# Optimization experiments

Hardware: AMD Instinct MI355X
Metric: run time of the kernel (lower is better)

Reference implementation:

```python
import jax, jax.numpy as jnp
import numpy as np

DIM = 384
HEADS = 6
N_TOKEN = 2240
HIDDEN = int(DIM * 4.0)
EPS = 1e-5


def layernorm(x, g, b):
    mu = jnp.mean(x, axis=-1, keepdims=True)
    var = jnp.mean(jnp.square(x - mu), axis=-1, keepdims=True)
    return (x - mu) * jax.lax.rsqrt(var + EPS) * g + b


def setup_inputs() -> dict:
    key = jax.random.key(0)
    ks = jax.random.split(key, 10)
    B, N, C = 2, 2240, DIM
    s = 0.02
    return {
        "x": jax.random.normal(ks[0], (B, N, C), dtype=jnp.float32),
        "encoder_pos": jax.random.normal(ks[1], (1, N_TOKEN, C), dtype=jnp.float32) * s,
        "ln1_g": jnp.ones((C,), jnp.float32),
        "ln1_b": jnp.zeros((C,), jnp.float32),
        "w_qkv": jax.random.normal(ks[2], (3 * C, C), dtype=jnp.float32) * s,  # torch Linear [out,in], no bias
        "w_proj": jax.random.normal(ks[3], (C, C), dtype=jnp.float32) * s,
        "b_proj": jnp.zeros((C,), jnp.float32),
        "ln2_g": jnp.ones((C,), jnp.float32),
        "ln2_b": jnp.zeros((C,), jnp.float32),
        "w_fc1": jax.random.normal(ks[4], (HIDDEN, C), dtype=jnp.float32) * s,
        "b_fc1": jnp.zeros((HIDDEN,), jnp.float32),
        "w_fc2": jax.random.normal(ks[5], (C, HIDDEN), dtype=jnp.float32) * s,
        "b_fc2": jnp.zeros((C,), jnp.float32),
    }


def reference(x, encoder_pos, ln1_g, ln1_b, w_qkv, w_proj, b_proj, ln2_g, ln2_b, w_fc1, b_fc1, w_fc2, b_fc2):
    B, N, C = x.shape
    H = HEADS
    hd = C // H
    scale = hd ** -0.5

    # positional embedding: each of the n_token rows repeated N//n_token times (contiguously)
    rep = N // encoder_pos.shape[1]
    pos = jnp.repeat(encoder_pos, rep, axis=1)  # [1, N, C]
    x = x + pos

    # attention
    h = layernorm(x, ln1_g, ln1_b)
    qkv = h @ w_qkv.T  # [B, N, 3C]
    qkv = qkv.reshape(B, N, 3, H, hd).transpose(2, 0, 3, 1, 4)  # [3, B, H, N, hd]
    q, k, v = qkv[0], qkv[1], qkv[2]
    attn = jax.nn.softmax(jnp.einsum("bhqd,bhkd->bhqk", q, k) * scale, axis=-1)  # [B, H, N, N]
    o = jnp.einsum("bhqk,bhkd->bhqd", attn, v).transpose(0, 2, 1, 3).reshape(B, N, C)
    o = o @ w_proj.T + b_proj
    x = x + o

    # MLP
    h = layernorm(x, ln2_g, ln2_b)
    h = jax.nn.gelu(h @ w_fc1.T + b_fc1, approximate=False)
    h = h @ w_fc2.T + b_fc2
    x = x + h
    return (x, attn)
```

## Files before the change

### kernel.cpp

```cpp
#include <hip/hip_runtime.h>
#include <math.h>

typedef unsigned short u16;
typedef unsigned int   u32;
typedef __attribute__((ext_vector_type(8))) short short8;
typedef __attribute__((ext_vector_type(4))) float floatx4;

#define MFMA16(a,b,c) __builtin_amdgcn_mfma_f32_16x16x32_bf16((a),(b),(c),0,0,0)

constexpr int BB  = 2;
constexpr int NT  = 2240;
constexpr int CD  = 384;
constexpr int NH  = 6;
constexpr int HD  = 64;
constexpr int HID = 1536;
constexpr int M   = BB * NT;
constexpr int CS  = 5;
constexpr int CTILES = NT / 64 / CS;
constexpr float SCALE = 0.125f;

__device__ inline u16 f2bf(float f) {
  u32 u = __float_as_uint(f);
  u = (u + 0x7fffu + ((u >> 16) & 1u)) >> 16;
  return (u16)u;
}
__device__ inline float bf2f(u16 b) { return __uint_as_float(((u32)b) << 16); }

__global__ void cvt_all(const float* __restrict__ s0, u16* __restrict__ d0, int n0_,
                        const float* __restrict__ s1, u16* __restrict__ d1, int n1_,
                        const float* __restrict__ s2, u16* __restrict__ d2, int n2_,
                        const float* __restrict__ s3, u16* __restrict__ d3, int n3_) {
  int i = (blockIdx.x * 256 + threadIdx.x) * 4;
  const float* s; u16* d; int base;
  if (i < n0_)                   { s = s0; d = d0; base = 0; }
  else if (i < n0_ + n1_)        { s = s1; d = d1; base = n0_; }
  else if (i < n0_ + n1_ + n2_)  { s = s2; d = d2; base = n0_ + n1_; }
  else                           { s = s3; d = d3; base = n0_ + n1_ + n2_; }
  int j = i - base;
  float4 v = *(const float4*)(s + j);
  ushort4 o; o.x = f2bf(v.x); o.y = f2bf(v.y); o.z = f2bf(v.z); o.w = f2bf(v.w);
  *(ushort4*)(d + j) = o;
}

__global__ __launch_bounds__(128) void ln_kernel(
    const float* __restrict__ xin, const float* __restrict__ pos,
    const float* __restrict__ g, const float* __restrict__ bta,
    float* __restrict__ x1out, u16* __restrict__ hout) {
  int row = blockIdx.x;
  int n = row % NT;
  int t = threadIdx.x;
  const float* xr = xin + (size_t)row * CD;
  float v[3], s1 = 0.f, s2 = 0.f;
  #pragma unroll
  for (int j = 0; j < 3; ++j) {
    int c = t + j * 128;
    float x = xr[c];
    if (pos) x += pos[(size_t)n * CD + c];
    v[j] = x; s1 += x; s2 += x * x;
  }
  #pragma unroll
  for (int off = 32; off; off >>= 1) { s1 += __shfl_down(s1, off); s2 += __shfl_down(s2, off); }
  __shared__ float rbuf[4];
  __shared__ float stats[2];
  int lane = t & 63, wid = t >> 6;
  if (lane == 0) { rbuf[wid] = s1; rbuf[2 + wid] = s2; }
  __syncthreads();
  if (t == 0) {
    float a = rbuf[0] + rbuf[1], b2 = rbuf[2] + rbuf[3];
    float mu = a / CD;
    float var = b2 / CD - mu * mu;
    stats[0] = mu; stats[1] = rsqrtf(var + 1e-5f);
  }
  __syncthreads();
  float mu = stats[0], rs = stats[1];
  #pragma unroll
  for (int j = 0; j < 3; ++j) {
    int c = t + j * 128;
    float h = (v[j] - mu) * rs * g[c] + bta[c];
    hout[(size_t)row * CD + c] = f2bf(h);
    if (x1out) x1out[(size_t)row * CD + c] = v[j];
  }
}

template <int EPI>
__global__ __launch_bounds__(256) void gemm_bt(
    const u16* __restrict__ A, const u16* __restrict__ Wt, int K,
    const float* __restrict__ bias, const float* __restrict__ res,
    float* __restrict__ outf, u16* __restrict__ outb,
    u16* __restrict__ qout, u16* __restrict__ kout, u16* __restrict__ vtout) {
  __shared__ __align__(16) u16 As[64][72];
  __shared__ __align__(16) u16 Bs[64][72];
  int m0 = blockIdx.y * 64, n0 = blockIdx.x * 64;
  int t = threadIdx.x;
  int lane = t & 63, w = t >> 6, wm = w & 1, wn = w >> 1;
  int quad = lane >> 4, c16 = lane & 15;
  int lrow = t >> 2, lseg = t & 3;
  const u16* ga = A + (size_t)(m0 + lrow) * K + lseg * 8;
  const u16* gb = Wt + (size_t)(n0 + lrow) * K + lseg * 8;
  floatx4 acc[2][2] = {};
  for (int k0 = 0; k0 < K; k0 += 64) {
    uint4 av0 = *(const uint4*)(ga + k0);
    uint4 av1 = *(const uint4*)(ga + k0 + 32);
    uint4 bv0 = *(const uint4*)(gb + k0);
    uint4 bv1 = *(const uint4*)(gb + k0 + 32);
    __syncthreads();
    *(uint4*)&As[lrow][lseg * 8] = av0;
    *(uint4*)&As[lrow][32 + lseg * 8] = av1;
    *(uint4*)&Bs[lrow][lseg * 8] = bv0;
    *(uint4*)&Bs[lrow][32 + lseg * 8] = bv1;
    __syncthreads();
    #pragma unroll
    for (int ks = 0; ks < 2; ++ks) {
      short8 af[2], bf[2];
      #pragma unroll
      for (int mt = 0; mt < 2; ++mt) af[mt] = *(const short8*)&As[wm * 32 + mt * 16 + c16][ks * 32 + quad * 8];
      #pragma unroll
      for (int nt = 0; nt < 2; ++nt) bf[nt] = *(const short8*)&Bs[wn * 32 + nt * 16 + c16][ks * 32 + quad * 8];
      #pragma unroll
      for (int mt = 0; mt < 2; ++mt)
        #pragma unroll
        for (int nt = 0; nt < 2; ++nt)
          acc[mt][nt] = MFMA16(af[mt], bf[nt], acc[mt][nt]);
    }
  }
  if (EPI == 0) {
    int s = n0 / 384;
    int hh = (n0 % 384) / 64;
    int b_ = m0 / NT, nn0 = m0 % NT;
    __syncthreads();
    #pragma unroll
    for (int mt = 0; mt < 2; ++mt)
      #pragma unroll
      for (int nt = 0; nt < 2; ++nt)
        #pragma unroll
        for (int r = 0; r < 4; ++r) {
          int m_l = wm * 32 + mt * 16 + quad * 4 + r;
          int d_l = wn * 32 + nt * 16 + c16;
          u16 bv = f2bf(acc[mt][nt][r]);
          if (s < 2) As[m_l][d_l] = bv;
          else       As[d_l][m_l] = bv;
        }
    __syncthreads();
    int row = t >> 2, cs0 = (t & 3) * 16;
    uint4 va = *(const uint4*)&As[row][cs0];
    uint4 vb = *(const uint4*)&As[row][cs0 + 8];
    u16* dst;
    if (s == 0)      dst = qout  + ((size_t)(b_ * NH + hh) * NT + nn0 + row) * HD + cs0;
    else if (s == 1) dst = kout  + ((size_t)(b_ * NH + hh) * NT + nn0 + row) * HD + cs0;
    else             dst = vtout + ((size_t)(b_ * NH + hh) * HD + row) * NT + nn0 + cs0;
    *(uint4*)dst = va;
    *(uint4*)(dst + 8) = vb;
  } else {
    #pragma unroll
    for (int mt = 0; mt < 2; ++mt) {
      #pragma unroll
      for (int nt = 0; nt < 2; ++nt) {
        int rg0 = m0 + wm * 32 + mt * 16 + quad * 4;
        int cg = n0 + wn * 32 + nt * 16 + c16;
        #pragma unroll
        for (int r = 0; r < 4; ++r) {
          float v = acc[mt][nt][r];
          int m = rg0 + r;
          if (EPI == 2) {
            v += bias[cg];
            v = 0.5f * v * (1.0f + erff(v * 0.70710678118f));
            outb[(size_t)m * HID + cg] = f2bf(v);
          } else {
            outf[(size_t)m * CD + cg] = v + bias[cg] + res[(size_t)m * CD + cg];
          }
        }
      }
    }
  }
}

__global__ __launch_bounds__(256) void attn_pass1(
    const u16* __restrict__ qb, const u16* __restrict__ kb, float* __restrict__ ml) {
  __shared__ __align__(16) u16 Ks[64][72];
  int bh = blockIdx.y, chunk = blockIdx.z;
  int q0 = blockIdx.x * 64;
  int t = threadIdx.x, w = t >> 6, lane = t & 63, quad = lane >> 4, c16 = lane & 15;
  int lrow = t >> 2, lseg = t & 3;

  const u16* qp = qb + ((size_t)bh * NT + q0 + w * 16 + c16) * HD;
  short8 qf0 = *(const short8*)(qp + quad * 8);
  short8 qf1 = *(const short8*)(qp + 32 + quad * 8);
  const u16* kbase = kb + (size_t)bh * NT * HD;

  float m_i[4], l_i[4];
  #pragma unroll
  for (int r = 0; r < 4; ++r) { m_i[r] = -1e30f; l_i[r] = 0.f; }

  for (int ct = 0; ct < CTILES; ++ct) {
    int col0 = (chunk * CTILES + ct) * 64;
    const u16* kg = kbase + (size_t)(col0 + lrow) * HD + lseg * 8;
    uint4 kv0 = *(const uint4*)kg;
    uint4 kv1 = *(const uint4*)(kg + 32);
    __syncthreads();
    *(uint4*)&Ks[lrow][lseg * 8] = kv0;
    *(uint4*)&Ks[lrow][32 + lseg * 8] = kv1;
    __syncthreads();
    floatx4 s_acc[4] = {};
    #pragma unroll
    for (int nt = 0; nt < 4; ++nt) {
      const u16* kp = &Ks[nt * 16 + c16][quad * 8];
      s_acc[nt] = MFMA16(qf0, *(const short8*)(kp), s_acc[nt]);
      s_acc[nt] = MFMA16(qf1, *(const short8*)(kp + 32), s_acc[nt]);
    }
    #pragma unroll
    for (int r = 0; r < 4; ++r) {
      float rm = fmaxf(fmaxf(s_acc[0][r], s_acc[1][r]), fmaxf(s_acc[2][r], s_acc[3][r])) * SCALE;
      #pragma unroll
      for (int off = 1; off < 16; off <<= 1) rm = fmaxf(rm, __shfl_xor(rm, off));
      float nm = fmaxf(m_i[r], rm);
      float ps = 0.f;
      #pragma unroll
      for (int nt = 0; nt < 4; ++nt) ps += __expf(s_acc[nt][r] * SCALE - nm);
      #pragma unroll
      for (int off = 1; off < 16; off <<= 1) ps += __shfl_xor(ps, off);
      l_i[r] = l_i[r] * __expf(m_i[r] - nm) + ps;
      m_i[r] = nm;
    }
  }
  if (c16 == 0) {
    #pragma unroll
    for (int r = 0; r < 4; ++r) {
      int row = q0 + w * 16 + quad * 4 + r;
      float* p = ml + ((size_t)(bh * NT + row) * CS + chunk) * 2;
      p[0] = m_i[r]; p[1] = l_i[r];
    }
  }
}

__global__ __launch_bounds__(256) void attn_pass2(
    const u16* __restrict__ qb, const u16* __restrict__ kb, const u16* __restrict__ vtb,
    const float* __restrict__ ml, float* __restrict__ attn_out, u16* __restrict__ o_part) {
  __shared__ __align__(16) u16 Ks[64][72];
  __shared__ __align__(16) u16 Vs[64][72];
  __shared__ __align__(16) u16 Plds[4][16][72];
  __shared__ float mfin[64], rlfin[64];
  int bh = blockIdx.y, chunk = blockIdx.z;
  int b = bh / NH, hh = bh % NH;
  int q0 = blockIdx.x * 64;
  int t = threadIdx.x, w = t >> 6, lane = t & 63, quad = lane >> 4, c16 = lane & 15;
  int lrow = t >> 2, lseg = t & 3;

  if (t < 64) {
    const float* p = ml + (size_t)(bh * NT + q0 + t) * CS * 2;
    float mm = -1e30f;
    #pragma unroll
    for (int c = 0; c < CS; ++c) mm = fmaxf(mm, p[c * 2]);
    float ll = 0.f;
    #pragma unroll
    for (int c = 0; c < CS; ++c) ll += p[c * 2 + 1] * __expf(p[c * 2] - mm);
    mfin[t] = mm; rlfin[t] = 1.0f / ll;
  }
  __syncthreads();
  float m_i[4], rl[4];
  #pragma unroll
  for (int r = 0; r < 4; ++r) {
    int rr = w * 16 + quad * 4 + r;
    m_i[r] = mfin[rr]; rl[r] = rlfin[rr];
  }

  const u16* qp = qb + ((size_t)bh * NT + q0 + w * 16 + c16) * HD;
  short8 qf0 = *(const short8*)(qp + quad * 8);
  short8 qf1 = *(const short8*)(qp + 32 + quad * 8);
  const u16* kbase = kb + (size_t)bh * NT * HD;
  const u16* vbase = vtb + (size_t)bh * HD * NT;

  floatx4 o_acc[4] = {};
  float* attn_bh = attn_out + (size_t)bh * NT * NT;
  for (int ct = 0; ct < CTILES; ++ct) {
    int col0 = (chunk * CTILES + ct) * 64;
    const u16* kg = kbase + (size_t)(col0 + lrow) * HD + lseg * 8;
    const u16* vg = vbase + (size_t)lrow * NT + col0 + lseg * 8;
    uint4 kv0 = *(const uint4*)kg;
    uint4 kv1 = *(const uint4*)(kg + 32);
    uint4 vv0 = *(const uint4*)vg;
    uint4 vv1 = *(const uint4*)(vg + 32);
    __syncthreads();
    *(uint4*)&Ks[lrow][lseg * 8] = kv0;
    *(uint4*)&Ks[lrow][32 + lseg * 8] = kv1;
    *(uint4*)&Vs[lrow][lseg * 8] = vv0;
    *(uint4*)&Vs[lrow][32 + lseg * 8] = vv1;
    __syncthreads();
    floatx4 s_acc[4] = {};
    #pragma unroll
    for (int nt = 0; nt < 4; ++nt) {
      const u16* kp = &Ks[nt * 16 + c16][quad * 8];
      s_acc[nt] = MFMA16(qf0, *(const short8*)(kp), s_acc[nt]);
      s_acc[nt] = MFMA16(qf1, *(const short8*)(kp + 32), s_acc[nt]);
    }
    #pragma unroll
    for (int nt = 0; nt < 4; ++nt) {
      #pragma unroll
      for (int r = 0; r < 4; ++r) {
        float p = __expf(s_acc[nt][r] * SCALE - m_i[r]) * rl[r];
        __builtin_nontemporal_store(
            p, &attn_bh[(size_t)(q0 + w * 16 + quad * 4 + r) * NT + col0 + nt * 16 + c16]);
        Plds[w][quad * 4 + r][nt * 16 + c16] = f2bf(p);
      }
    }
    #pragma unroll
    for (int ks = 0; ks < 2; ++ks) {
      short8 pa = *(const short8*)&Plds[w][c16][ks * 32 + quad * 8];
      #pragma unroll
      for (int dt = 0; dt < 4; ++dt) {
        short8 vb = *(const short8*)&Vs[dt * 16 + c16][ks * 32 + quad * 8];
        o_acc[dt] = MFMA16(pa, vb, o_acc[dt]);
      }
    }
  }
  #pragma unroll
  for (int dt = 0; dt < 4; ++dt) {
    #pragma unroll
    for (int r = 0; r < 4; ++r) {
      int m = b * NT + q0 + w * 16 + quad * 4 + r;
      int cc = hh * 64 + dt * 16 + c16;
      o_part[((size_t)chunk * M + m) * CD + cc] = f2bf(o_acc[dt][r]);
    }
  }
}

__global__ void osum_kernel(const u16* __restrict__ o_part, u16* __restrict__ o_bf) {
  int i = (blockIdx.x * 256 + threadIdx.x) * 4;
  float4 s = {0.f, 0.f, 0.f, 0.f};
  #pragma unroll
  for (int c = 0; c < CS; ++c) {
    ushort4 v = *(const ushort4*)(o_part + (size_t)c * M * CD + i);
    s.x += bf2f(v.x); s.y += bf2f(v.y); s.z += bf2f(v.z); s.w += bf2f(v.w);
  }
  ushort4 o; o.x = f2bf(s.x); o.y = f2bf(s.y); o.z = f2bf(s.z); o.w = f2bf(s.w);
  *(ushort4*)(o_bf + i) = o;
}

extern "C" void kernel_launch(void* const* d_in, const int* in_sizes, int n_in,
                              void* d_out, int out_size, void* d_ws, size_t ws_size,
                              hipStream_t stream) {
  const float* x      = (const float*)d_in[0];
  const float* pos    = (const float*)d_in[1];
  const float* ln1_g  = (const float*)d_in[2];
  const float* ln1_b  = (const float*)d_in[3];
  const float* w_qkv  = (const float*)d_in[4];
  const float* w_proj = (const float*)d_in[5];
  const float* b_proj = (const float*)d_in[6];
  const float* ln2_g  = (const float*)d_in[7];
  const float* ln2_b  = (const float*)d_in[8];
  const float* w_fc1  = (const float*)d_in[9];
  const float* b_fc1  = (const float*)d_in[10];
  const float* w_fc2  = (const float*)d_in[11];
  const float* b_fc2  = (const float*)d_in[12];

  float* out      = (float*)d_out;
  float* attn_out = out + (size_t)M * CD;

  char* ws = (char*)d_ws;
  size_t o = 0;
  auto carve = [&](size_t bytes) { char* p = ws + o; o += bytes; return p; };
  float* x1    = (float*)carve((size_t)M * CD * 4);
  u16* h1      = (u16*)carve((size_t)M * CD * 2);
  u16* wqkv_b  = (u16*)carve((size_t)3 * CD * CD * 2);
  u16* wproj_b = (u16*)carve((size_t)CD * CD * 2);
  u16* wfc1_b  = (u16*)carve((size_t)HID * CD * 2);
  u16* wfc2_b  = (u16*)carve((size_t)CD * HID * 2);
  u16* q_bf    = (u16*)carve((size_t)BB * NH * NT * HD * 2);
  u16* k_bf    = (u16*)carve((size_t)BB * NH * NT * HD * 2);
  u16* vt_bf   = (u16*)carve((size_t)BB * NH * NT * HD * 2);
  u16* o_bf    = (u16*)carve((size_t)M * CD * 2);
  float* x2    = (float*)carve((size_t)M * CD * 4);
  u16* h2      = (u16*)carve((size_t)M * CD * 2);
  u16* g_bf    = (u16*)carve((size_t)M * HID * 2);
  float* ml    = (float*)carve((size_t)NH * BB * NT * CS * 2 * 4);
  u16* o_part  = (u16*)carve((size_t)CS * M * CD * 2);
  (void)ws_size; (void)in_sizes; (void)n_in; (void)out_size;

  constexpr int NQ = 3 * CD * CD, NP = CD * CD, N1 = HID * CD, N2 = CD * HID;
  cvt_all<<<(NQ + NP + N1 + N2) / 1024, 256, 0, stream>>>(
      w_qkv, wqkv_b, NQ, w_proj, wproj_b, NP, w_fc1, wfc1_b, N1, w_fc2, wfc2_b, N2);

  ln_kernel<<<M, 128, 0, stream>>>(x, pos, ln1_g, ln1_b, x1, h1);

  gemm_bt<0><<<dim3((3 * CD) / 64, M / 64), 256, 0, stream>>>(
      h1, wqkv_b, CD, nullptr, nullptr, nullptr, nullptr, q_bf, k_bf, vt_bf);

  attn_pass1<<<dim3(NT / 64, BB * NH, CS), 256, 0, stream>>>(q_bf, k_bf, ml);
  attn_pass2<<<dim3(NT / 64, BB * NH, CS), 256, 0, stream>>>(q_bf, k_bf, vt_bf, ml, attn_out, o_part);
  osum_kernel<<<(M * CD) / 1024, 256, 0, stream>>>(o_part, o_bf);

  gemm_bt<3><<<dim3(CD / 64, M / 64), 256, 0, stream>>>(
      o_bf, wproj_b, CD, b_proj, x1, x2, nullptr, nullptr, nullptr, nullptr);
  ln_kernel<<<M, 128, 0, stream>>>(x2, nullptr, ln2_g, ln2_b, nullptr, h2);

  gemm_bt<2><<<dim3(HID / 64, M / 64), 256, 0, stream>>>(
      h2, wfc1_b, CD, b_fc1, nullptr, nullptr, g_bf, nullptr, nullptr, nullptr);

  gemm_bt<3><<<dim3(CD / 64, M / 64), 256, 0, stream>>>(
      g_bf, wfc2_b, HID, b_fc2, x2, out, nullptr, nullptr, nullptr, nullptr);
}
```

Measured before the change: 430.6 us.

## Fuse weight conversion into LN, fold partial-O sum into proj GEMM, prefetch tiles

Merges the weight fp32-to-bf16 conversion into the first layernorm launch as extra blocks. Removes the separate partial-output summation kernel by summing the five attention chunk partials inside the projection GEMM's A-tile load. Adds register prefetch of the next K/V or A/B tile in the GEMM and both attention passes. Pass1 swaps MFMA operand order so each lane holds a single query row's statistics, cutting the shuffle reductions. These changes remove launches and a memory round trip, at the cost of five times the A loads and more register pressure in the projection GEMM.

```diff
diff --git a/kernel.cpp b/kernel.cpp
--- a/kernel.cpp
+++ b/kernel.cpp
@@ -26,28 +26,82 @@
 }
 __device__ inline float bf2f(u16 b) { return __uint_as_float(((u32)b) << 16); }
 
-__global__ void cvt_all(const float* __restrict__ s0, u16* __restrict__ d0, int n0_,
-                        const float* __restrict__ s1, u16* __restrict__ d1, int n1_,
-                        const float* __restrict__ s2, u16* __restrict__ d2, int n2_,
-                        const float* __restrict__ s3, u16* __restrict__ d3, int n3_) {
-  int i = (blockIdx.x * 256 + threadIdx.x) * 4;
-  const float* s; u16* d; int base;
-  if (i < n0_)                   { s = s0; d = d0; base = 0; }
-  else if (i < n0_ + n1_)        { s = s1; d = d1; base = n0_; }
-  else if (i < n0_ + n1_ + n2_)  { s = s2; d = d2; base = n0_ + n1_; }
-  else                           { s = s3; d = d3; base = n0_ + n1_ + n2_; }
-  int j = i - base;
-  float4 v = *(const float4*)(s + j);
-  ushort4 o; o.x = f2bf(v.x); o.y = f2bf(v.y); o.z = f2bf(v.z); o.w = f2bf(v.w);
-  *(ushort4*)(d + j) = o;
-}
-
-__global__ __launch_bounds__(128) void ln_kernel(
+__device__ inline uint4 sum5_bf(uint4 a0, uint4 a1, uint4 a2, uint4 a3, uint4 a4) {
+  union U { uint4 v; u16 h[8]; };
+  U u0, u1, u2, u3, u4, o;
+  u0.v = a0; u1.v = a1; u2.v = a2; u3.v = a3; u4.v = a4;
+  #pragma unroll
+  for (int e = 0; e < 8; ++e) {
+    float f = bf2f(u0.h[e]) + bf2f(u1.h[e]) + bf2f(u2.h[e]) + bf2f(u3.h[e]) + bf2f(u4.h[e]);
+    o.h[e] = f2bf(f);
+  }
+  return o.v;
+}
+
+constexpr int NQ = 3 * CD * CD, NP = CD * CD, N1 = HID * CD, N2 = CD * HID;
+constexpr int CVT_BLOCKS = (NQ + NP + N1 + N2) / 512;
+
+__global__ __launch_bounds__(128) void ln_cvt_kernel(
     const float* __restrict__ xin, const float* __restrict__ pos,
     const float* __restrict__ g, const float* __restrict__ bta,
-    float* __restrict__ x1out, u16* __restrict__ hout) {
+    float* __restrict__ x1out, u16* __restrict__ hout,
+    const float* __restrict__ s0, u16* __restrict__ d0,
+    const float* __restrict__ s1, u16* __restrict__ d1,
+    const float* __restrict__ s2, u16* __restrict__ d2,
+    const float* __restrict__ s3, u16* __restrict__ d3) {
+  int t = threadIdx.x;
+  if (blockIdx.x >= M) {
+    int i = ((blockIdx.x - M) * 128 + t) * 4;
+    const float* s; u16* d; int base;
+    if (i < NQ)                { s = s0; d = d0; base = 0; }
+    else if (i < NQ + NP)      { s = s1; d = d1; base = NQ; }
+    else if (i < NQ + NP + N1) { s = s2; d = d2; base = NQ + NP; }
+    else                       { s = s3; d = d3; base = NQ + NP + N1; }
+    int j = i - base;
+    float4 v = *(const float4*)(s + j);
+    ushort4 o; o.x = f2bf(v.x); o.y = f2bf(v.y); o.z = f2bf(v.z); o.w = f2bf(v.w);
+    *(ushort4*)(d + j) = o;
+    return;
+  }
   int row = blockIdx.x;
   int n = row % NT;
+  const float* xr = xin + (size_t)row * CD;
+  float v[3], s1v = 0.f, s2v = 0.f;
+  #pragma unroll
+  for (int j = 0; j < 3; ++j) {
+    int c = t + j * 128;
+    float x = xr[c] + pos[(size_t)n * CD + c];
+    v[j] = x; s1v += x; s2v += x * x;
+  }
+  #pragma unroll
+  for (int off = 32; off; off >>= 1) { s1v += __shfl_down(s1v, off); s2v += __shfl_down(s2v, off); }
+  __shared__ float rbuf[4];
+  __shared__ float stats[2];
+  int lane = t & 63, wid = t >> 6;
+  if (lane == 0) { rbuf[wid] = s1v; rbuf[2 + wid] = s2v; }
+  __syncthreads();
+  if (t == 0) {
+    float a = rbuf[0] + rbuf[1], b2 = rbuf[2] + rbuf[3];
+    float mu = a / CD;
+    float var = b2 / CD - mu * mu;
+    stats[0] = mu; stats[1] = rsqrtf(var + 1e-5f);
+  }
+  __syncthreads();
+  float mu = stats[0], rs = stats[1];
+  #pragma unroll
+  for (int j = 0; j < 3; ++j) {
+    int c = t + j * 128;
+    float h = (v[j] - mu) * rs * g[c] + bta[c];
+    hout[(size_t)row * CD + c] = f2bf(h);
+    x1out[(size_t)row * CD + c] = v[j];
+  }
+}
+
+__global__ __launch_bounds__(128) void ln_kernel(
+    const float* __restrict__ xin,
+    const float* __restrict__ g, const float* __restrict__ bta,
+    u16* __restrict__ hout) {
+  int row = blockIdx.x;
   int t = threadIdx.x;
   const float* xr = xin + (size_t)row * CD;
   float v[3], s1 = 0.f, s2 = 0.f;
@@ -55,7 +109,6 @@
   for (int j = 0; j < 3; ++j) {
     int c = t + j * 128;
     float x = xr[c];
-    if (pos) x += pos[(size_t)n * CD + c];
     v[j] = x; s1 += x; s2 += x * x;
   }
   #pragma unroll
@@ -76,13 +129,11 @@
   #pragma unroll
   for (int j = 0; j < 3; ++j) {
     int c = t + j * 128;
-    float h = (v[j] - mu) * rs * g[c] + bta[c];
-    hout[(size_t)row * CD + c] = f2bf(h);
-    if (x1out) x1out[(size_t)row * CD + c] = v[j];
-  }
-}
-
-template <int EPI>
+    hout[(size_t)row * CD + c] = f2bf((v[j] - mu) * rs * g[c] + bta[c]);
+  }
+}
+
+template <int EPI, bool OSUM>
 __global__ __launch_bounds__(256) void gemm_bt(
     const u16* __restrict__ A, const u16* __restrict__ Wt, int K,
     const float* __restrict__ bias, const float* __restrict__ res,
@@ -95,20 +146,39 @@
   int lane = t & 63, w = t >> 6, wm = w & 1, wn = w >> 1;
   int quad = lane >> 4, c16 = lane & 15;
   int lrow = t >> 2, lseg = t & 3;
-  const u16* ga = A + (size_t)(m0 + lrow) * K + lseg * 8;
+  constexpr int SL = OSUM ? 5 : 1;
+  const u16* ga[SL];
+  #pragma unroll
+  for (int s = 0; s < SL; ++s)
+    ga[s] = A + (size_t)s * M * CD + (size_t)(m0 + lrow) * K + lseg * 8;
   const u16* gb = Wt + (size_t)(n0 + lrow) * K + lseg * 8;
   floatx4 acc[2][2] = {};
+  uint4 av0[SL], av1[SL], bv0, bv1;
+  #pragma unroll
+  for (int s = 0; s < SL; ++s) { av0[s] = *(const uint4*)(ga[s]); av1[s] = *(const uint4*)(ga[s] + 32); }
+  bv0 = *(const uint4*)(gb);
+  bv1 = *(const uint4*)(gb + 32);
   for (int k0 = 0; k0 < K; k0 += 64) {
-    uint4 av0 = *(const uint4*)(ga + k0);
-    uint4 av1 = *(const uint4*)(ga + k0 + 32);
-    uint4 bv0 = *(const uint4*)(gb + k0);
-    uint4 bv1 = *(const uint4*)(gb + k0 + 32);
-    __syncthreads();
-    *(uint4*)&As[lrow][lseg * 8] = av0;
-    *(uint4*)&As[lrow][32 + lseg * 8] = av1;
+    __syncthreads();
+    uint4 wa0, wa1;
+    if (OSUM) {
+      wa0 = sum5_bf(av0[0], av0[1], av0[2], av0[3], av0[4 % SL]);
+      wa1 = sum5_bf(av1[0], av1[1], av1[2], av1[3], av1[4 % SL]);
+    } else { wa0 = av0[0]; wa1 = av1[0]; }
+    *(uint4*)&As[lrow][lseg * 8] = wa0;
+    *(uint4*)&As[lrow][32 + lseg * 8] = wa1;
     *(uint4*)&Bs[lrow][lseg * 8] = bv0;
     *(uint4*)&Bs[lrow][32 + lseg * 8] = bv1;
     __syncthreads();
+    if (k0 + 64 < K) {
+      #pragma unroll
+      for (int s = 0; s < SL; ++s) {
+        av0[s] = *(const uint4*)(ga[s] + k0 + 64);
+        av1[s] = *(const uint4*)(ga[s] + k0 + 96);
+      }
+      bv0 = *(const uint4*)(gb + k0 + 64);
+      bv1 = *(const uint4*)(gb + k0 + 96);
+    }
     #pragma unroll
     for (int ks = 0; ks < 2; ++ks) {
       short8 af[2], bf[2];
@@ -187,48 +257,52 @@
   short8 qf1 = *(const short8*)(qp + 32 + quad * 8);
   const u16* kbase = kb + (size_t)bh * NT * HD;
 
-  float m_i[4], l_i[4];
-  #pragma unroll
-  for (int r = 0; r < 4; ++r) { m_i[r] = -1e30f; l_i[r] = 0.f; }
+  float m_i = -1e30f, l_i = 0.f;
+
+  const u16* kg = kbase + (size_t)(chunk * CTILES * 64 + lrow) * HD + lseg * 8;
+  uint4 kv0 = *(const uint4*)kg;
+  uint4 kv1 = *(const uint4*)(kg + 32);
 
   for (int ct = 0; ct < CTILES; ++ct) {
-    int col0 = (chunk * CTILES + ct) * 64;
-    const u16* kg = kbase + (size_t)(col0 + lrow) * HD + lseg * 8;
-    uint4 kv0 = *(const uint4*)kg;
-    uint4 kv1 = *(const uint4*)(kg + 32);
     __syncthreads();
     *(uint4*)&Ks[lrow][lseg * 8] = kv0;
     *(uint4*)&Ks[lrow][32 + lseg * 8] = kv1;
     __syncthreads();
+    if (ct + 1 < CTILES) {
+      const u16* kn = kbase + (size_t)((chunk * CTILES + ct + 1) * 64 + lrow) * HD + lseg * 8;
+      kv0 = *(const uint4*)kn;
+      kv1 = *(const uint4*)(kn + 32);
+    }
     floatx4 s_acc[4] = {};
     #pragma unroll
     for (int nt = 0; nt < 4; ++nt) {
       const u16* kp = &Ks[nt * 16 + c16][quad * 8];
-      s_acc[nt] = MFMA16(qf0, *(const short8*)(kp), s_acc[nt]);
-      s_acc[nt] = MFMA16(qf1, *(const short8*)(kp + 32), s_acc[nt]);
-    }
-    #pragma unroll
-    for (int r = 0; r < 4; ++r) {
-      float rm = fmaxf(fmaxf(s_acc[0][r], s_acc[1][r]), fmaxf(s_acc[2][r], s_acc[3][r])) * SCALE;
-      #pragma unroll
-      for (int off = 1; off < 16; off <<= 1) rm = fmaxf(rm, __shfl_xor(rm, off));
-      float nm = fmaxf(m_i[r], rm);
-      float ps = 0.f;
-      #pragma unroll
-      for (int nt = 0; nt < 4; ++nt) ps += __expf(s_acc[nt][r] * SCALE - nm);
-      #pragma unroll
-      for (int off = 1; off < 16; off <<= 1) ps += __shfl_xor(ps, off);
-      l_i[r] = l_i[r] * __expf(m_i[r] - nm) + ps;
-      m_i[r] = nm;
-    }
-  }
-  if (c16 == 0) {
-    #pragma unroll
-    for (int r = 0; r < 4; ++r) {
-      int row = q0 + w * 16 + quad * 4 + r;
-      float* p = ml + ((size_t)(bh * NT + row) * CS + chunk) * 2;
-      p[0] = m_i[r]; p[1] = l_i[r];
-    }
+      s_acc[nt] = MFMA16(*(const short8*)(kp), qf0, s_acc[nt]);
+      s_acc[nt] = MFMA16(*(const short8*)(kp + 32), qf1, s_acc[nt]);
+    }
+    float rm = -1e30f;
+    #pragma unroll
+    for (int nt = 0; nt < 4; ++nt)
+      #pragma unroll
+      for (int r = 0; r < 4; ++r) rm = fmaxf(rm, s_acc[nt][r]);
+    rm *= SCALE;
+    rm = fmaxf(rm, __shfl_xor(rm, 16));
+    rm = fmaxf(rm, __shfl_xor(rm, 32));
+    float nm = fmaxf(m_i, rm);
+    float ps = 0.f;
+    #pragma unroll
+    for (int nt = 0; nt < 4; ++nt)
+      #pragma unroll
+      for (int r = 0; r < 4; ++r) ps += __expf(s_acc[nt][r] * SCALE - nm);
+    ps += __shfl_xor(ps, 16);
+    ps += __shfl_xor(ps, 32);
+    l_i = l_i * __expf(m_i - nm) + ps;
+    m_i = nm;
+  }
+  if (quad == 0) {
+    int row = q0 + w * 16 + c16;
+    float* p = ml + ((size_t)(bh * NT + row) * CS + chunk) * 2;
+    p[0] = m_i; p[1] = l_i;
   }
 }
 
@@ -245,6 +319,17 @@
   int t = threadIdx.x, w = t >> 6, lane = t & 63, quad = lane >> 4, c16 = lane & 15;
   int lrow = t >> 2, lseg = t & 3;
 
+  const u16* kbase = kb + (size_t)bh * NT * HD;
+  const u16* vbase = vtb + (size_t)bh * HD * NT;
+
+  int col00 = chunk * CTILES * 64;
+  const u16* kg = kbase + (size_t)(col00 + lrow) * HD + lseg * 8;
+  const u16* vg = vbase + (size_t)lrow * NT + col00 + lseg * 8;
+  uint4 kv0 = *(const uint4*)kg;
+  uint4 kv1 = *(const uint4*)(kg + 32);
+  uint4 vv0 = *(const uint4*)vg;
+  uint4 vv1 = *(const uint4*)(vg + 32);
+
   if (t < 64) {
     const float* p = ml + (size_t)(bh * NT + q0 + t) * CS * 2;
     float mm = -1e30f;
@@ -266,25 +351,26 @@
   const u16* qp = qb + ((size_t)bh * NT + q0 + w * 16 + c16) * HD;
   short8 qf0 = *(const short8*)(qp + quad * 8);
   short8 qf1 = *(const short8*)(qp + 32 + quad * 8);
-  const u16* kbase = kb + (size_t)bh * NT * HD;
-  const u16* vbase = vtb + (size_t)bh * HD * NT;
 
   floatx4 o_acc[4] = {};
   float* attn_bh = attn_out + (size_t)bh * NT * NT;
   for (int ct = 0; ct < CTILES; ++ct) {
     int col0 = (chunk * CTILES + ct) * 64;
-    const u16* kg = kbase + (size_t)(col0 + lrow) * HD + lseg * 8;
-    const u16* vg = vbase + (size_t)lrow * NT + col0 + lseg * 8;
-    uint4 kv0 = *(const uint4*)kg;
-    uint4 kv1 = *(const uint4*)(kg + 32);
-    uint4 vv0 = *(const uint4*)vg;
-    uint4 vv1 = *(const uint4*)(vg + 32);
     __syncthreads();
     *(uint4*)&Ks[lrow][lseg * 8] = kv0;
     *(uint4*)&Ks[lrow][32 + lseg * 8] = kv1;
     *(uint4*)&Vs[lrow][lseg * 8] = vv0;
     *(uint4*)&Vs[lrow][32 + lseg * 8] = vv1;
     __syncthreads();
+    if (ct + 1 < CTILES) {
+      int coln = col0 + 64;
+      const u16* kn = kbase + (size_t)(coln + lrow) * HD + lseg * 8;
+      const u16* vn = vbase + (size_t)lrow * NT + coln + lseg * 8;
+      kv0 = *(const uint4*)kn;
+      kv1 = *(const uint4*)(kn + 32);
+      vv0 = *(const uint4*)vn;
+      vv1 = *(const uint4*)(vn + 32);
+    }
     floatx4 s_acc[4] = {};
     #pragma unroll
     for (int nt = 0; nt < 4; ++nt) {
@@ -321,18 +407,6 @@
       o_part[((size_t)chunk * M + m) * CD + cc] = f2bf(o_acc[dt][r]);
     }
   }
-}
-
-__global__ void osum_kernel(const u16* __restrict__ o_part, u16* __restrict__ o_bf) {
-  int i = (blockIdx.x * 256 + threadIdx.x) * 4;
-  float4 s = {0.f, 0.f, 0.f, 0.f};
-  #pragma unroll
-  for (int c = 0; c < CS; ++c) {
-    ushort4 v = *(const ushort4*)(o_part + (size_t)c * M * CD + i);
-    s.x += bf2f(v.x); s.y += bf2f(v.y); s.z += bf2f(v.z); s.w += bf2f(v.w);
-  }
-  ushort4 o; o.x = f2bf(s.x); o.y = f2bf(s.y); o.z = f2bf(s.z); o.w = f2bf(s.w);
-  *(ushort4*)(o_bf + i) = o;
 }
 
 extern "C" void kernel_launch(void* const* d_in, const int* in_sizes, int n_in,
@@ -367,7 +441,6 @@
   u16* q_bf    = (u16*)carve((size_t)BB * NH * NT * HD * 2);
   u16* k_bf    = (u16*)carve((size_t)BB * NH * NT * HD * 2);
   u16* vt_bf   = (u16*)carve((size_t)BB * NH * NT * HD * 2);
-  u16* o_bf    = (u16*)carve((size_t)M * CD * 2);
   float* x2    = (float*)carve((size_t)M * CD * 4);
   u16* h2      = (u16*)carve((size_t)M * CD * 2);
   u16* g_bf    = (u16*)carve((size_t)M * HID * 2);
@@ -375,26 +448,23 @@
   u16* o_part  = (u16*)carve((size_t)CS * M * CD * 2);
   (void)ws_size; (void)in_sizes; (void)n_in; (void)out_size;
 
-  constexpr int NQ = 3 * CD * CD, NP = CD * CD, N1 = HID * CD, N2 = CD * HID;
-  cvt_all<<<(NQ + NP + N1 + N2) / 1024, 256, 0, stream>>>(
-      w_qkv, wqkv_b, NQ, w_proj, wproj_b, NP, w_fc1, wfc1_b, N1, w_fc2, wfc2_b, N2);
-
-  ln_kernel<<<M, 128, 0, stream>>>(x, pos, ln1_g, ln1_b, x1, h1);
-
-  gemm_bt<0><<<dim3((3 * CD) / 64, M / 64), 256, 0, stream>>>(
+  ln_cvt_kernel<<<M + CVT_BLOCKS, 128, 0, stream>>>(
+      x, pos, ln1_g, ln1_b, x1, h1,
+      w_qkv, wqkv_b, w_proj, wproj_b, w_fc1, wfc1_b, w_fc2, wfc2_b);
+
+  gemm_bt<0, false><<<dim3((3 * CD) / 64, M / 64), 256, 0, stream>>>(
       h1, wqkv_b, CD, nullptr, nullptr, nullptr, nullptr, q_bf, k_bf, vt_bf);
 
   attn_pass1<<<dim3(NT / 64, BB * NH, CS), 256, 0, stream>>>(q_bf, k_bf, ml);
   attn_pass2<<<dim3(NT / 64, BB * NH, CS), 256, 0, stream>>>(q_bf, k_bf, vt_bf, ml, attn_out, o_part);
-  osum_kernel<<<(M * CD) / 1024, 256, 0, stream>>>(o_part, o_bf);
-
-  gemm_bt<3><<<dim3(CD / 64, M / 64), 256, 0, stream>>>(
-      o_bf, wproj_b, CD, b_proj, x1, x2, nullptr, nullptr, nullptr, nullptr);
-  ln_kernel<<<M, 128, 0, stream>>>(x2, nullptr, ln2_g, ln2_b, nullptr, h2);
-
-  gemm_bt<2><<<dim3(HID / 64, M / 64), 256, 0, stream>>>(
+
+  gemm_bt<3, true><<<dim3(CD / 64, M / 64), 256, 0, stream>>>(
+      o_part, wproj_b, CD, b_proj, x1, x2, nullptr, nullptr, nullptr, nullptr);
+  ln_kernel<<<M, 128, 0, stream>>>(x2, ln2_g, ln2_b, h2);
+
+  gemm_bt<2, false><<<dim3(HID / 64, M / 64), 256, 0, stream>>>(
       h2, wfc1_b, CD, b_fc1, nullptr, nullptr, g_bf, nullptr, nullptr, nullptr);
 
-  gemm_bt<3><<<dim3(CD / 64, M / 64), 256, 0, stream>>>(
+  gemm_bt<3, false><<<dim3(CD / 64, M / 64), 256, 0, stream>>>(
       g_bf, wfc2_b, HID, b_fc2, x2, out, nullptr, nullptr, nullptr, nullptr);
 }
```

New measurement: 410.8 us (median of 2 runs). 4.6% less time.
